# Kernel optimization log

Hardware: AMD Instinct MI355X
Metric: run time of the kernel (lower is better)

Reference implementation:

```python
import jax, jax.numpy as jnp
import numpy as np

# Dimensions
B, T, S, V, CV, D = 32, 128, 400, 32000, 600, 512
PAD = 1  # vocabs['code'].stoi['<blank>']


def setup_inputs() -> dict:
    key = jax.random.key(0)
    k0, k1, k2, k3, k4 = jax.random.split(key, 5)
    hidden = jax.random.normal(k0, (B * T, D), dtype=jnp.float32)
    # attention weights: normalized over source length
    copy_attn = jax.nn.softmax(jax.random.normal(k1, (B * T, S), dtype=jnp.float32), axis=-1)
    # src_map: one-hot scatter matrix [B, S, CV] mapping src positions to extended-vocab ids
    src_ids = jax.random.randint(k2, (B, S), 0, CV)
    src_map = jax.nn.one_hot(src_ids, CV, dtype=jnp.float32)
    W = jax.random.normal(k3, (V, D), dtype=jnp.float32) * 0.02
    b = jnp.zeros((V,), dtype=jnp.float32)
    w_copy = jax.random.normal(k4, (D,), dtype=jnp.float32) * 0.02
    b_copy = jnp.zeros((), dtype=jnp.float32)
    return {"hidden": hidden, "copy_attn": copy_attn, "src_map": src_map,
            "W": W, "b": b, "w_copy": w_copy, "b_copy": b_copy}


def reference(hidden, copy_attn, src_map, W, b, w_copy, b_copy):
    # logits over target vocab, pad logit masked to -inf
    logits = hidden @ W.T + b                      # [B*T, V]
    logits = logits.at[:, PAD].set(-jnp.inf)
    prob = jax.nn.softmax(logits, axis=-1)         # [B*T, V]
    # copy gate p(z)
    copy = jax.nn.sigmoid(hidden @ w_copy + b_copy)[:, None]  # [B*T, 1]
    out_prob = prob * (1.0 - copy)                 # generation branch
    mul_attn = copy_attn * copy                    # copy branch, [B*T, S]
    # scatter attention mass into extended vocab via one-hot bmm
    copy_prob = jnp.einsum('bts,bsv->btv', mul_attn.reshape(B, T, S), src_map)
    copy_prob = copy_prob.reshape(-1, src_map.shape[-1])  # [B*T, CV]
    return jnp.concatenate([out_prob, copy_prob], axis=1)  # [B*T, V+CV]
```

## Files before the change

### kernel.cpp

```cpp
#include <hip/hip_runtime.h>
#include <hip/hip_bf16.h>
#include <cstdint>
#include <cstddef>

#define M_ROWS   4096
#define N_VOCAB  32000
#define K_DIM    512
#define S_DIM    400
#define CV_DIM   600
#define OUT_PITCH 32600
#define PAD_IDX  1

typedef __attribute__((ext_vector_type(8))) short short8;
typedef __attribute__((ext_vector_type(8))) unsigned short ushort8;
typedef __attribute__((ext_vector_type(4))) float f32x4;

#define WB_OFF   0ull
#define HB_OFF   32768000ull
#define COPYG_OFF 36962304ull
#define RSUM_OFF  36978688ull
#define SSCALE_OFF 36995072ull
#define SRCID_OFF 37011456ull
#define EB_OFF    37062656ull
#define WS_NEED_BF16 (EB_OFF + 262144000ull)

__device__ inline void gload_lds16(const void* g, void* l) {
  __builtin_amdgcn_global_load_lds(
      (const __attribute__((address_space(1))) unsigned int*)g,
      (__attribute__((address_space(3))) unsigned int*)l, 16, 0, 0);
}

__device__ inline unsigned short f32_to_bf16_rn(float f) {
  unsigned u = __float_as_uint(f);
  u += 0x7FFFu + ((u >> 16) & 1u);
  return (unsigned short)(u >> 16);
}
__device__ inline float bf16_to_f32(unsigned short h) {
  return __uint_as_float((unsigned)h << 16);
}

__global__ void cvt_kernel(const float4* __restrict__ in, ushort4* __restrict__ out, unsigned n4) {
  unsigned stride = gridDim.x * blockDim.x;
  for (unsigned i = blockIdx.x * blockDim.x + threadIdx.x; i < n4; i += stride) {
    float4 v = in[i];
    ushort4 o;
    o.x = f32_to_bf16_rn(v.x);
    o.y = f32_to_bf16_rn(v.y);
    o.z = f32_to_bf16_rn(v.z);
    o.w = f32_to_bf16_rn(v.w);
    out[i] = o;
  }
}

__global__ void copygate_cvt_kernel(const float* __restrict__ hidden,
                                    const float* __restrict__ w_copy,
                                    const float* __restrict__ b_copy,
                                    float* __restrict__ copyg,
                                    unsigned short* __restrict__ Hb) {
  unsigned gw = (blockIdx.x * blockDim.x + threadIdx.x) >> 6;
  unsigned lane = threadIdx.x & 63u;
  if (gw >= M_ROWS) return;
  const float4* h4 = (const float4*)(hidden + (size_t)gw * K_DIM);
  const float4* w4 = (const float4*)w_copy;
  float4 a0 = h4[lane * 2 + 0], w0 = w4[lane * 2 + 0];
  float4 a1 = h4[lane * 2 + 1], w1 = w4[lane * 2 + 1];
  float dot = a0.x * w0.x + a0.y * w0.y + a0.z * w0.z + a0.w * w0.w
            + a1.x * w1.x + a1.y * w1.y + a1.z * w1.z + a1.w * w1.w;
  ushort8 hb;
  hb[0] = f32_to_bf16_rn(a0.x); hb[1] = f32_to_bf16_rn(a0.y);
  hb[2] = f32_to_bf16_rn(a0.z); hb[3] = f32_to_bf16_rn(a0.w);
  hb[4] = f32_to_bf16_rn(a1.x); hb[5] = f32_to_bf16_rn(a1.y);
  hb[6] = f32_to_bf16_rn(a1.z); hb[7] = f32_to_bf16_rn(a1.w);
  *(ushort8*)(Hb + (size_t)gw * K_DIM + lane * 8u) = hb;
  #pragma unroll
  for (int mask = 1; mask < 64; mask <<= 1) dot += __shfl_xor(dot, mask);
  if (lane == 0) copyg[gw] = 1.f / (1.f + __expf(-(dot + b_copy[0])));
}

__global__ void srcids_kernel(const float* __restrict__ src_map, int* __restrict__ src_ids) {
  unsigned pos = (blockIdx.x * blockDim.x + threadIdx.x) >> 6;
  unsigned lane = threadIdx.x & 63u;
  if (pos >= 32 * S_DIM) return;
  const float* row = src_map + (size_t)pos * CV_DIM;
  int found = 1 << 30;
  for (int v = lane; v < CV_DIM; v += 64)
    if (row[v] > 0.5f) found = v;
  #pragma unroll
  for (int mask = 1; mask < 64; mask <<= 1) {
    int o = __shfl_xor(found, mask);
    found = found < o ? found : o;
  }
  if (lane == 0) src_ids[pos] = found;
}

template<int BF16OUT>
__global__ __launch_bounds__(256, 4)
void gemm_exp_kernel(const unsigned short* __restrict__ A,
                     const unsigned short* __restrict__ B,
                     const float* __restrict__ bias,
                     float* __restrict__ out,
                     unsigned short* __restrict__ Eb,
                     float* __restrict__ row_sum) {
  __shared__ unsigned short smem[16384];
  unsigned short* As = smem;
  unsigned short* Bs = smem + 8192;

  unsigned bid = blockIdx.x;
  unsigned wg = (bid & 7u) * 1000u + (bid >> 3);
  unsigned mt = wg / 250u, nt = wg % 250u;
  unsigned m0 = mt * 128u, n0 = nt * 128u;
  unsigned tid = threadIdx.x;
  unsigned lane = tid & 63u;
  unsigned wid = tid >> 6;
  unsigned wm = wid >> 1, wn = wid & 1u;
  unsigned lr = lane >> 4, lc = lane & 15u;

  const unsigned ch0 = (lr ^ (lc & 7u)) * 8u;
  const unsigned ch1 = ((lr + 4u) ^ (lc & 7u)) * 8u;

  const unsigned short* Asrc[4];
  const unsigned short* Bsrc[4];
  unsigned dst[4];
  #pragma unroll
  for (unsigned i = 0; i < 4; ++i) {
    unsigned u = i * 256u + tid;
    unsigned rr = u >> 3;
    unsigned ch = (u & 7u) ^ (rr & 7u);
    dst[i] = u * 16u;
    Asrc[i] = A + (size_t)(m0 + rr) * K_DIM + ch * 8u;
    Bsrc[i] = B + (size_t)(n0 + rr) * K_DIM + ch * 8u;
  }
  unsigned arow[4], brow[4];
  #pragma unroll
  for (int m = 0; m < 4; ++m) arow[m] = (wm * 64u + m * 16u + lc) * 64u;
  #pragma unroll
  for (int n = 0; n < 4; ++n) brow[n] = (wn * 64u + n * 16u + lc) * 64u;

  f32x4 acc[4][4] = {};

  for (unsigned kt = 0; kt < 8; ++kt) {
    unsigned k0 = kt * 64u;
    #pragma unroll
    for (unsigned i = 0; i < 4; ++i) {
      gload_lds16(Asrc[i] + k0, (char*)As + dst[i]);
      gload_lds16(Bsrc[i] + k0, (char*)Bs + dst[i]);
    }
    __syncthreads();
    {
      short8 af[4][2], bf[4][2];
      #pragma unroll
      for (int m = 0; m < 4; ++m) {
        af[m][0] = *(const short8*)&As[arow[m] + ch0];
        af[m][1] = *(const short8*)&As[arow[m] + ch1];
      }
      #pragma unroll
      for (int n = 0; n < 4; ++n) {
        bf[n][0] = *(const short8*)&Bs[brow[n] + ch0];
        bf[n][1] = *(const short8*)&Bs[brow[n] + ch1];
      }
      #pragma unroll
      for (int ks = 0; ks < 2; ++ks)
        #pragma unroll
        for (int m = 0; m < 4; ++m)
          #pragma unroll
          for (int n = 0; n < 4; ++n)
            acc[m][n] = __builtin_amdgcn_mfma_f32_16x16x32_bf16(bf[n][ks], af[m][ks],
                                                                acc[m][n], 0, 0, 0);
    }
    __syncthreads();
  }

  float4 bv4[4];
  #pragma unroll
  for (int n = 0; n < 4; ++n)
    bv4[n] = *(const float4*)&bias[n0 + wn * 64u + n * 16u + lr * 4u];

  if (BF16OUT) {
    #pragma unroll
    for (int m = 0; m < 4; ++m) {
      unsigned grow = m0 + wm * 64u + m * 16u + lc;
      unsigned short* rowp = Eb + (size_t)grow * N_VOCAB;
      #pragma unroll
      for (int n = 0; n < 4; ++n) {
        unsigned gcol = n0 + wn * 64u + n * 16u + lr * 4u;
        float e0 = (gcol + 0u == PAD_IDX) ? 0.f : __expf(acc[m][n][0] + bv4[n].x);
        float e1 = (gcol + 1u == PAD_IDX) ? 0.f : __expf(acc[m][n][1] + bv4[n].y);
        float e2 = (gcol + 2u == PAD_IDX) ? 0.f : __expf(acc[m][n][2] + bv4[n].z);
        float e3 = (gcol + 3u == PAD_IDX) ? 0.f : __expf(acc[m][n][3] + bv4[n].w);
        ushort4 o;
        o.x = f32_to_bf16_rn(e0); o.y = f32_to_bf16_rn(e1);
        o.z = f32_to_bf16_rn(e2); o.w = f32_to_bf16_rn(e3);
        *(ushort4*)(rowp + gcol) = o;
      }
    }
  } else {
    #pragma unroll
    for (int m = 0; m < 4; ++m) {
      unsigned grow = m0 + wm * 64u + m * 16u + lc;
      float rs = 0.f;
      #pragma unroll
      for (int n = 0; n < 4; ++n) {
        unsigned gcol = n0 + wn * 64u + n * 16u + lr * 4u;
        float4 e;
        e.x = (gcol + 0u == PAD_IDX) ? 0.f : __expf(acc[m][n][0] + bv4[n].x);
        e.y = (gcol + 1u == PAD_IDX) ? 0.f : __expf(acc[m][n][1] + bv4[n].y);
        e.z = (gcol + 2u == PAD_IDX) ? 0.f : __expf(acc[m][n][2] + bv4[n].z);
        e.w = (gcol + 3u == PAD_IDX) ? 0.f : __expf(acc[m][n][3] + bv4[n].w);
        *(float4*)(out + (size_t)grow * OUT_PITCH + gcol) = e;
        rs += e.x + e.y + e.z + e.w;
      }
      rs += __shfl_xor(rs, 16);
      rs += __shfl_xor(rs, 32);
      if (lr == 0) atomicAdd(&row_sum[grow], rs);
    }
  }
}

__global__ __launch_bounds__(256)
void norm_scale_kernel(const unsigned short* __restrict__ Eb,
                       const float* __restrict__ copyg,
                       float* __restrict__ out) {
  unsigned r = blockIdx.x;
  unsigned tid = threadIdx.x;
  const ushort8* src = (const ushort8*)(Eb + (size_t)r * N_VOCAB);
  ushort8 v[16];
  float lsum = 0.f;
  #pragma unroll
  for (int i = 0; i < 16; ++i) {
    unsigned c = (unsigned)i * 256u + tid;
    if (c < 4000u) {
      v[i] = src[c];
      #pragma unroll
      for (int k = 0; k < 8; ++k) lsum += bf16_to_f32(v[i][k]);
    }
  }
  #pragma unroll
  for (int mask = 1; mask < 64; mask <<= 1) lsum += __shfl_xor(lsum, mask);
  __shared__ float wsum[4];
  if ((tid & 63u) == 0) wsum[tid >> 6] = lsum;
  __syncthreads();
  float s = (1.f - copyg[r]) / (wsum[0] + wsum[1] + wsum[2] + wsum[3]);
  float* dst = out + (size_t)r * OUT_PITCH;
  #pragma unroll
  for (int i = 0; i < 16; ++i) {
    unsigned c = (unsigned)i * 256u + tid;
    if (c < 4000u) {
      float4 lo, hi;
      lo.x = bf16_to_f32(v[i][0]) * s; lo.y = bf16_to_f32(v[i][1]) * s;
      lo.z = bf16_to_f32(v[i][2]) * s; lo.w = bf16_to_f32(v[i][3]) * s;
      hi.x = bf16_to_f32(v[i][4]) * s; hi.y = bf16_to_f32(v[i][5]) * s;
      hi.z = bf16_to_f32(v[i][6]) * s; hi.w = bf16_to_f32(v[i][7]) * s;
      float4* o = (float4*)(dst + c * 8u);
      o[0] = lo; o[1] = hi;
    }
  }
}

__global__ void finalize_kernel(const float* __restrict__ row_sum, const float* __restrict__ copyg,
                                float* __restrict__ sscale) {
  unsigned r = blockIdx.x * blockDim.x + threadIdx.x;
  if (r < M_ROWS) sscale[r] = (1.f - copyg[r]) / row_sum[r];
}

__global__ void scale_kernel(float4* __restrict__ out, const float* __restrict__ sscale) {
  const unsigned total = M_ROWS * (N_VOCAB / 4);
  unsigned stride = gridDim.x * blockDim.x;
  for (unsigned i = blockIdx.x * blockDim.x + threadIdx.x; i < total; i += stride) {
    unsigned r = i / (N_VOCAB / 4);
    unsigned c = i % (N_VOCAB / 4);
    float s = sscale[r];
    float4 v = out[(size_t)r * (OUT_PITCH / 4) + c];
    v.x *= s; v.y *= s; v.z *= s; v.w *= s;
    out[(size_t)r * (OUT_PITCH / 4) + c] = v;
  }
}

__global__ void copyprob_kernel(const float* __restrict__ attn, const int* __restrict__ src_ids,
                                const float* __restrict__ copyg, float* __restrict__ out) {
  unsigned r = blockIdx.x;
  unsigned tid = threadIdx.x;
  __shared__ float cp[CV_DIM];
  for (unsigned v = tid; v < CV_DIM; v += 128) cp[v] = 0.f;
  __syncthreads();
  unsigned batch = r >> 7;
  float g = copyg[r];
  for (unsigned s = tid; s < S_DIM; s += 128) {
    float a = attn[(size_t)r * S_DIM + s] * g;
    atomicAdd(&cp[src_ids[batch * S_DIM + s]], a);
  }
  __syncthreads();
  for (unsigned v = tid; v < CV_DIM; v += 128)
    out[(size_t)r * OUT_PITCH + N_VOCAB + v] = cp[v];
}

extern "C" void kernel_launch(void* const* d_in, const int* in_sizes, int n_in,
                              void* d_out, int out_size, void* d_ws, size_t ws_size,
                              hipStream_t stream) {
  const float* hidden    = (const float*)d_in[0];
  const float* copy_attn = (const float*)d_in[1];
  const float* src_map   = (const float*)d_in[2];
  const float* W         = (const float*)d_in[3];
  const float* bias      = (const float*)d_in[4];
  const float* w_copy    = (const float*)d_in[5];
  const float* b_copy    = (const float*)d_in[6];
  float* out = (float*)d_out;

  char* ws = (char*)d_ws;
  unsigned short* Wb = (unsigned short*)(ws + WB_OFF);
  unsigned short* Hb = (unsigned short*)(ws + HB_OFF);
  float* copyg   = (float*)(ws + COPYG_OFF);
  float* row_sum = (float*)(ws + RSUM_OFF);
  float* sscale  = (float*)(ws + SSCALE_OFF);
  int*   src_ids = (int*)(ws + SRCID_OFF);
  unsigned short* Eb = (unsigned short*)(ws + EB_OFF);

  const bool bf16_path = (ws_size >= WS_NEED_BF16);

  cvt_kernel<<<2048, 256, 0, stream>>>((const float4*)W, (ushort4*)Wb,
                                       (unsigned)(N_VOCAB * K_DIM / 4));
  copygate_cvt_kernel<<<M_ROWS / 4, 256, 0, stream>>>(hidden, w_copy, b_copy, copyg, Hb);
  srcids_kernel<<<(32 * S_DIM) / 4, 256, 0, stream>>>(src_map, src_ids);

  if (bf16_path) {
    gemm_exp_kernel<1><<<(M_ROWS / 128) * (N_VOCAB / 128), 256, 0, stream>>>(
        Hb, Wb, bias, out, Eb, row_sum);
    norm_scale_kernel<<<M_ROWS, 256, 0, stream>>>(Eb, copyg, out);
  } else {
    hipMemsetAsync(row_sum, 0, M_ROWS * sizeof(float), stream);
    gemm_exp_kernel<0><<<(M_ROWS / 128) * (N_VOCAB / 128), 256, 0, stream>>>(
        Hb, Wb, bias, out, Eb, row_sum);
    finalize_kernel<<<(M_ROWS + 255) / 256, 256, 0, stream>>>(row_sum, copyg, sscale);
    scale_kernel<<<4096, 256, 0, stream>>>((float4*)out, sscale);
  }

  copyprob_kernel<<<M_ROWS, 128, 0, stream>>>(copy_attn, src_ids, copyg, out);
}
```

Before: 411.9 us.

## Make GEMM persistent with full A slab resident in LDS and B read from global

New measurement: 713.0 us. +73.1%, slower.

```diff
diff --git a/kernel.cpp b/kernel.cpp
--- a/kernel.cpp
+++ b/kernel.cpp
@@ -94,69 +94,65 @@
 }
 
 template<int BF16OUT>
-__global__ __launch_bounds__(256, 4)
+__global__ __launch_bounds__(512, 1)
 void gemm_exp_kernel(const unsigned short* __restrict__ A,
                      const unsigned short* __restrict__ B,
                      const float* __restrict__ bias,
                      float* __restrict__ out,
                      unsigned short* __restrict__ Eb,
                      float* __restrict__ row_sum) {
-  __shared__ unsigned short smem[16384];
-  unsigned short* As = smem;
-  unsigned short* Bs = smem + 8192;
+  __shared__ unsigned short As[128 * 512];
 
   unsigned bid = blockIdx.x;
-  unsigned wg = (bid & 7u) * 1000u + (bid >> 3);
-  unsigned mt = wg / 250u, nt = wg % 250u;
-  unsigned m0 = mt * 128u, n0 = nt * 128u;
+  unsigned nrange = bid & 7u;
+  unsigned slab = bid >> 3;
+  unsigned m0 = slab * 128u;
+  unsigned t0 = (nrange * 125u) >> 3;
+  unsigned t1 = ((nrange + 1u) * 125u) >> 3;
+
   unsigned tid = threadIdx.x;
   unsigned lane = tid & 63u;
   unsigned wid = tid >> 6;
-  unsigned wm = wid >> 1, wn = wid & 1u;
+  unsigned wm = wid >> 2, wn = wid & 3u;
   unsigned lr = lane >> 4, lc = lane & 15u;
 
-  const unsigned ch0 = (lr ^ (lc & 7u)) * 8u;
-  const unsigned ch1 = ((lr + 4u) ^ (lc & 7u)) * 8u;
-
-  const unsigned short* Asrc[4];
-  const unsigned short* Bsrc[4];
-  unsigned dst[4];
-  #pragma unroll
-  for (unsigned i = 0; i < 4; ++i) {
-    unsigned u = i * 256u + tid;
-    unsigned rr = u >> 3;
-    unsigned ch = (u & 7u) ^ (rr & 7u);
-    dst[i] = u * 16u;
-    Asrc[i] = A + (size_t)(m0 + rr) * K_DIM + ch * 8u;
-    Bsrc[i] = B + (size_t)(n0 + rr) * K_DIM + ch * 8u;
-  }
-  unsigned arow[4], brow[4];
-  #pragma unroll
-  for (int m = 0; m < 4; ++m) arow[m] = (wm * 64u + m * 16u + lc) * 64u;
-  #pragma unroll
-  for (int n = 0; n < 4; ++n) brow[n] = (wn * 64u + n * 16u + lc) * 64u;
-
-  f32x4 acc[4][4] = {};
-
-  for (unsigned kt = 0; kt < 8; ++kt) {
-    unsigned k0 = kt * 64u;
+  #pragma unroll
+  for (unsigned i = 0; i < 16; ++i) {
+    unsigned u = i * 512u + tid;
+    unsigned row = u >> 6;
+    unsigned c = u & 63u;
+    unsigned cs = c ^ (row & 7u);
+    gload_lds16(A + (size_t)(m0 + row) * K_DIM + cs * 8u, (char*)As + (size_t)u * 16u);
+  }
+  asm volatile("s_waitcnt vmcnt(0)" ::: "memory");
+  __syncthreads();
+
+  unsigned arow[4];
+  #pragma unroll
+  for (int m = 0; m < 4; ++m) arow[m] = (wm * 64u + m * 16u + lc) * 512u;
+  const unsigned chk0 = ((0u * 4u + lr) ^ (lc & 7u)) * 8u;
+  const unsigned chk1 = ((1u * 4u + lr) ^ (lc & 7u)) * 8u;
+
+  for (unsigned t = t0; t < t1; ++t) {
+    unsigned n0 = t * 256u;
+    const unsigned short* Bn[4];
     #pragma unroll
-    for (unsigned i = 0; i < 4; ++i) {
-      gload_lds16(Asrc[i] + k0, (char*)As + dst[i]);
-      gload_lds16(Bsrc[i] + k0, (char*)Bs + dst[i]);
-    }
-    __syncthreads();
-    {
+    for (int n = 0; n < 4; ++n)
+      Bn[n] = B + (size_t)(n0 + wn * 64u + n * 16u + lc) * K_DIM + lr * 8u;
+
+    f32x4 acc[4][4] = {};
+    #pragma unroll
+    for (unsigned kt = 0; kt < 8; ++kt) {
       short8 af[4][2], bf[4][2];
       #pragma unroll
+      for (int n = 0; n < 4; ++n) {
+        bf[n][0] = *(const short8*)(Bn[n] + kt * 64u);
+        bf[n][1] = *(const short8*)(Bn[n] + kt * 64u + 32u);
+      }
+      #pragma unroll
       for (int m = 0; m < 4; ++m) {
-        af[m][0] = *(const short8*)&As[arow[m] + ch0];
-        af[m][1] = *(const short8*)&As[arow[m] + ch1];
-      }
-      #pragma unroll
-      for (int n = 0; n < 4; ++n) {
-        bf[n][0] = *(const short8*)&Bs[brow[n] + ch0];
-        bf[n][1] = *(const short8*)&Bs[brow[n] + ch1];
+        af[m][0] = *(const short8*)&As[arow[m] + kt * 64u + chk0];
+        af[m][1] = *(const short8*)&As[arow[m] + kt * 64u + chk1];
       }
       #pragma unroll
       for (int ks = 0; ks < 2; ++ks)
@@ -164,54 +160,53 @@
         for (int m = 0; m < 4; ++m)
           #pragma unroll
           for (int n = 0; n < 4; ++n)
-            acc[m][n] = __builtin_amdgcn_mfma_f32_16x16x32_bf16(bf[n][ks], af[m][ks],
-                                                                acc[m][n], 0, 0, 0);
+            acc[m][n] = __builtin_amdgcn_mfma_f32_16x16x32_bf16(
+                ks ? bf[n][1] : bf[n][0], ks ? af[m][1] : af[m][0], acc[m][n], 0, 0, 0);
     }
-    __syncthreads();
-  }
-
-  float4 bv4[4];
-  #pragma unroll
-  for (int n = 0; n < 4; ++n)
-    bv4[n] = *(const float4*)&bias[n0 + wn * 64u + n * 16u + lr * 4u];
-
-  if (BF16OUT) {
+
+    float4 bv4[4];
     #pragma unroll
-    for (int m = 0; m < 4; ++m) {
-      unsigned grow = m0 + wm * 64u + m * 16u + lc;
-      unsigned short* rowp = Eb + (size_t)grow * N_VOCAB;
-      #pragma unroll
-      for (int n = 0; n < 4; ++n) {
-        unsigned gcol = n0 + wn * 64u + n * 16u + lr * 4u;
-        float e0 = (gcol + 0u == PAD_IDX) ? 0.f : __expf(acc[m][n][0] + bv4[n].x);
-        float e1 = (gcol + 1u == PAD_IDX) ? 0.f : __expf(acc[m][n][1] + bv4[n].y);
-        float e2 = (gcol + 2u == PAD_IDX) ? 0.f : __expf(acc[m][n][2] + bv4[n].z);
-        float e3 = (gcol + 3u == PAD_IDX) ? 0.f : __expf(acc[m][n][3] + bv4[n].w);
-        ushort4 o;
-        o.x = f32_to_bf16_rn(e0); o.y = f32_to_bf16_rn(e1);
-        o.z = f32_to_bf16_rn(e2); o.w = f32_to_bf16_rn(e3);
-        *(ushort4*)(rowp + gcol) = o;
+    for (int n = 0; n < 4; ++n)
+      bv4[n] = *(const float4*)&bias[n0 + wn * 64u + n * 16u + lr * 4u];
+
+    if (BF16OUT) {
+      #pragma unroll
+      for (int m = 0; m < 4; ++m) {
+        unsigned grow = m0 + wm * 64u + m * 16u + lc;
+        unsigned short* rowp = Eb + (size_t)grow * N_VOCAB;
+        #pragma unroll
+        for (int n = 0; n < 4; ++n) {
+          unsigned gcol = n0 + wn * 64u + n * 16u + lr * 4u;
+          float e0 = (gcol + 0u == PAD_IDX) ? 0.f : __expf(acc[m][n][0] + bv4[n].x);
+          float e1 = (gcol + 1u == PAD_IDX) ? 0.f : __expf(acc[m][n][1] + bv4[n].y);
+          float e2 = (gcol + 2u == PAD_IDX) ? 0.f : __expf(acc[m][n][2] + bv4[n].z);
+          float e3 = (gcol + 3u == PAD_IDX) ? 0.f : __expf(acc[m][n][3] + bv4[n].w);
+          ushort4 o;
+          o.x = f32_to_bf16_rn(e0); o.y = f32_to_bf16_rn(e1);
+          o.z = f32_to_bf16_rn(e2); o.w = f32_to_bf16_rn(e3);
+          *(ushort4*)(rowp + gcol) = o;
+        }
       }
-    }
-  } else {
-    #pragma unroll
-    for (int m = 0; m < 4; ++m) {
-      unsigned grow = m0 + wm * 64u + m * 16u + lc;
-      float rs = 0.f;
-      #pragma unroll
-      for (int n = 0; n < 4; ++n) {
-        unsigned gcol = n0 + wn * 64u + n * 16u + lr * 4u;
-        float4 e;
-        e.x = (gcol + 0u == PAD_IDX) ? 0.f : __expf(acc[m][n][0] + bv4[n].x);
-        e.y = (gcol + 1u == PAD_IDX) ? 0.f : __expf(acc[m][n][1] + bv4[n].y);
-        e.z = (gcol + 2u == PAD_IDX) ? 0.f : __expf(acc[m][n][2] + bv4[n].z);
-        e.w = (gcol + 3u == PAD_IDX) ? 0.f : __expf(acc[m][n][3] + bv4[n].w);
-        *(float4*)(out + (size_t)grow * OUT_PITCH + gcol) = e;
-        rs += e.x + e.y + e.z + e.w;
+    } else {
+      #pragma unroll
+      for (int m = 0; m < 4; ++m) {
+        unsigned grow = m0 + wm * 64u + m * 16u + lc;
+        float rs = 0.f;
+        #pragma unroll
+        for (int n = 0; n < 4; ++n) {
+          unsigned gcol = n0 + wn * 64u + n * 16u + lr * 4u;
+          float4 e;
+          e.x = (gcol + 0u == PAD_IDX) ? 0.f : __expf(acc[m][n][0] + bv4[n].x);
+          e.y = (gcol + 1u == PAD_IDX) ? 0.f : __expf(acc[m][n][1] + bv4[n].y);
+          e.z = (gcol + 2u == PAD_IDX) ? 0.f : __expf(acc[m][n][2] + bv4[n].z);
+          e.w = (gcol + 3u == PAD_IDX) ? 0.f : __expf(acc[m][n][3] + bv4[n].w);
+          *(float4*)(out + (size_t)grow * OUT_PITCH + gcol) = e;
+          rs += e.x + e.y + e.z + e.w;
+        }
+        rs += __shfl_xor(rs, 16);
+        rs += __shfl_xor(rs, 32);
+        if (lr == 0) atomicAdd(&row_sum[grow], rs);
       }
-      rs += __shfl_xor(rs, 16);
-      rs += __shfl_xor(rs, 32);
-      if (lr == 0) atomicAdd(&row_sum[grow], rs);
     }
   }
 }
@@ -322,13 +317,11 @@
   srcids_kernel<<<(32 * S_DIM) / 4, 256, 0, stream>>>(src_map, src_ids);
 
   if (bf16_path) {
-    gemm_exp_kernel<1><<<(M_ROWS / 128) * (N_VOCAB / 128), 256, 0, stream>>>(
-        Hb, Wb, bias, out, Eb, row_sum);
+    gemm_exp_kernel<1><<<256, 512, 0, stream>>>(Hb, Wb, bias, out, Eb, row_sum);
     norm_scale_kernel<<<M_ROWS, 256, 0, stream>>>(Eb, copyg, out);
   } else {
     hipMemsetAsync(row_sum, 0, M_ROWS * sizeof(float), stream);
-    gemm_exp_kernel<0><<<(M_ROWS / 128) * (N_VOCAB / 128), 256, 0, stream>>>(
-        Hb, Wb, bias, out, Eb, row_sum);
+    gemm_exp_kernel<0><<<256, 512, 0, stream>>>(Hb, Wb, bias, out, Eb, row_sum);
     finalize_kernel<<<(M_ROWS + 255) / 256, 256, 0, stream>>>(row_sum, copyg, sscale);
     scale_kernel<<<4096, 256, 0, stream>>>((float4*)out, sscale);
   }
```
